# Optimization experiments

Measured on AMD Instinct MI355X. Metric: run time of the kernel, lower is better.

## Reference

```python
import jax, jax.numpy as jnp
import numpy as np

B, C, CI, HM, HC = 4, 64, 32, 128, 64  # batch, in_channels, inter_channels, main HW, cross HW
BN_EPS = 1e-5


def conv1x1(x, w, b):
    # x: [B,Cin,H,W], w: [Cout,Cin], b: [Cout]
    return jnp.einsum('bchw,oc->bohw', x, w) + b[None, :, None, None]


def _lin_coords(n_in, n_out):
    # PyTorch bilinear, align_corners=False: src = (i+0.5)*scale - 0.5, clamped
    scale = n_in / n_out
    src = (jnp.arange(n_out, dtype=jnp.float32) + 0.5) * scale - 0.5
    src = jnp.clip(src, 0.0, n_in - 1)
    i0 = jnp.floor(src).astype(jnp.int32)
    i1 = jnp.minimum(i0 + 1, n_in - 1)
    w = src - i0.astype(jnp.float32)
    return i0, i1, w


def resize_bilinear(x, h_out, w_out):
    # x: [B,C,H,W] -> [B,C,h_out,w_out], matches torch F.interpolate(mode='bilinear', align_corners=False)
    _, _, h_in, w_in = x.shape
    i0, i1, wh = _lin_coords(h_in, h_out)
    x = x[:, :, i0, :] * (1.0 - wh)[None, None, :, None] + x[:, :, i1, :] * wh[None, None, :, None]
    j0, j1, ww = _lin_coords(w_in, w_out)
    x = x[:, :, :, j0] * (1.0 - ww)[None, None, None, :] + x[:, :, :, j1] * ww[None, None, None, :]
    return x


def setup_inputs() -> dict:
    key = jax.random.key(0)
    ks = jax.random.split(key, 12)
    p = lambda k, shape, s=0.05: jax.random.normal(k, shape, dtype=jnp.float32) * s
    return {
        'main_feature': jax.random.normal(ks[0], (B, C, HM, HM), dtype=jnp.float32),
        'cross_feature': jax.random.normal(ks[1], (B, C, HC, HC), dtype=jnp.float32),
        'g_w': p(ks[2], (CI, C)), 'g_b': p(ks[3], (CI,)),
        'theta_w': p(ks[4], (CI, C)), 'theta_b': p(ks[5], (CI,)),
        'phi_w': p(ks[6], (CI, C)), 'phi_b': p(ks[7], (CI,)),
        'w_w': p(ks[8], (C, CI)), 'w_b': p(ks[9], (C,)),
        'bn_gamma': 1.0 + p(ks[10], (C,)), 'bn_beta': p(ks[11], (C,)),
    }


def reference(main_feature, cross_feature, g_w, g_b, theta_w, theta_b,
              phi_w, phi_b, w_w, w_b, bn_gamma, bn_beta):
    b, _, hc, wc = cross_feature.shape
    hm = main_feature.shape[2]
    # g(cross) -> [B, Nc, Ci]
    x = conv1x1(cross_feature, g_w, g_b).reshape(b, CI, -1).transpose(0, 2, 1)
    # theta(cross) -> [B, Ci, Nc]
    y = conv1x1(cross_feature, theta_w, theta_b).reshape(b, CI, -1)
    # phi(resize(main -> cross size)) -> [B, Nc, Ci]
    z = resize_bilinear(main_feature, hc, hc)
    z = conv1x1(z, phi_w, phi_b).reshape(b, CI, -1).transpose(0, 2, 1)
    # unscaled attention: [B, Nc, Nc]
    f = jnp.einsum('bnc,bcm->bnm', x, y)
    attn = jax.nn.softmax(f, axis=-1)
    out = jnp.einsum('bnm,bmc->bnc', attn, z)           # [B, Nc, Ci]
    out = out.transpose(0, 2, 1).reshape(b, CI, hc, wc)  # [B, Ci, Hc, Wc]
    # W: 1x1 conv + BatchNorm2d (training mode: batch statistics, biased var)
    out = conv1x1(out, w_w, w_b)
    mean = out.mean(axis=(0, 2, 3), keepdims=True)
    var = out.var(axis=(0, 2, 3), keepdims=True)
    out = (out - mean) * jax.lax.rsqrt(var + BN_EPS)
    out = out * bn_gamma[None, :, None, None] + bn_beta[None, :, None, None]
    out = resize_bilinear(out, hm, hm)
    return out + main_feature
```

## Files before the change

kernel.cpp:

```cpp
#include <hip/hip_runtime.h>
#include <hip/hip_bf16.h>


typedef __attribute__((ext_vector_type(8))) short bf16x8;
typedef __attribute__((ext_vector_type(4))) float f32x4;
typedef __attribute__((ext_vector_type(16))) float f32x16;

#define LOG2E 1.4426950408889634f

static __device__ __forceinline__ unsigned short f2bf_bits(float x) {
    __hip_bfloat16 h = __float2bfloat16(x);
    return *(unsigned short*)&h;
}
static __device__ __forceinline__ unsigned int pk2bf(float a, float b) {
    __hip_bfloat162 h = __float22bfloat162_rn(make_float2(a, b));
    return *(unsigned int*)&h;
}

static __device__ __forceinline__ void softmax_pack(
    const f32x16& s, float& den, bf16x8& ap1, bf16x8& ap2)
{
    float e[16];
#pragma unroll
    for (int r = 0; r < 16; ++r) e[r] = __builtin_amdgcn_exp2f(s[r]);
    den += (((e[0]+e[1])+(e[2]+e[3])) + ((e[4]+e[5])+(e[6]+e[7])))
         + (((e[8]+e[9])+(e[10]+e[11])) + ((e[12]+e[13])+(e[14]+e[15])));
    uint4 t1 = make_uint4(pk2bf(e[0],e[1]), pk2bf(e[2],e[3]),
                          pk2bf(e[4],e[5]), pk2bf(e[6],e[7]));
    uint4 t2 = make_uint4(pk2bf(e[8],e[9]), pk2bf(e[10],e[11]),
                          pk2bf(e[12],e[13]), pk2bf(e[14],e[15]));
    ap1 = *(bf16x8*)&t1; ap2 = *(bf16x8*)&t2;
}

__global__ __launch_bounds__(256) void qkv_kernel(
    const float* __restrict__ cross, const float* __restrict__ mainf,
    const float* __restrict__ g_w,  const float* __restrict__ g_b,
    const float* __restrict__ th_w, const float* __restrict__ th_b,
    const float* __restrict__ ph_w, const float* __restrict__ ph_b,
    __hip_bfloat16* __restrict__ Qb, __hip_bfloat16* __restrict__ Kf,
    __hip_bfloat16* __restrict__ Vf)
{
    __shared__ float xs[64][128];
    const int kind = blockIdx.x >> 7;
    const int sub  = blockIdx.x & 127;
    const int b    = sub >> 5;
    const int n0   = (sub & 31) << 7;
    const int tid  = threadIdx.x;
    const float* w  = (kind == 0) ? g_w : (kind == 1) ? th_w : ph_w;
    const float* bs = (kind == 0) ? g_b : (kind == 1) ? th_b : ph_b;

    if (kind < 2) {
        const float* src = cross + (((size_t)(b * 64)) << 12) + n0;
        const int jr = (tid & 31) << 2, c0 = tid >> 5;
#pragma unroll
        for (int it = 0; it < 8; ++it) {
            int c = (it << 3) | c0;
            *(float4*)&xs[c][jr] = *(const float4*)(src + ((size_t)c << 12) + jr);
        }
    } else {
        const int px = tid & 127, chh = tid >> 7;
        const int n = n0 + px;
        const int i2 = (n >> 6) << 1, j2 = (n & 63) << 1;
        const float* src = mainf + (((size_t)(b * 64)) << 14) + i2 * 128 + j2;
#pragma unroll 4
        for (int cc = 0; cc < 32; ++cc) {
            int c = (chh << 5) | cc;
            const float2 a = *(const float2*)(src + ((size_t)c << 14));
            const float2 d = *(const float2*)(src + ((size_t)c << 14) + 128);
            xs[c][px] = 0.25f * ((a.x + a.y) + (d.x + d.y));
        }
    }
    __syncthreads();

    const int px = tid & 127, cih = tid >> 7, ci0 = cih << 4;
    float acc[16];
#pragma unroll
    for (int j = 0; j < 16; ++j) acc[j] = bs[ci0 + j];
#pragma unroll 4
    for (int c = 0; c < 64; ++c) {
        float x = xs[c][px];
#pragma unroll
        for (int j = 0; j < 16; ++j)
            acc[j] = fmaf(w[((ci0 + j) << 6) + c], x, acc[j]);
    }
    const int n = n0 + px;
    const int chunk = n >> 5, kk = n & 31;
    if (kind == 0) {
#pragma unroll
        for (int j = 0; j < 16; ++j) acc[j] *= LOG2E;
        unsigned int u[8];
#pragma unroll
        for (int i = 0; i < 8; ++i)
            u[i] = (unsigned int)f2bf_bits(acc[2 * i]) |
                   ((unsigned int)f2bf_bits(acc[2 * i + 1]) << 16);
        uint4* d4 = (uint4*)(Qb + (size_t)((b << 12) + n) * 32 + ci0);
        d4[0] = make_uint4(u[0], u[1], u[2], u[3]);
        d4[1] = make_uint4(u[4], u[5], u[6], u[7]);
    } else if (kind == 1) {
        unsigned int u[8];
#pragma unroll
        for (int i = 0; i < 8; ++i)
            u[i] = (unsigned int)f2bf_bits(acc[2 * i]) |
                   ((unsigned int)f2bf_bits(acc[2 * i + 1]) << 16);
        const int q = (kk & ~12) | ((kk & 4) << 1) | ((kk & 8) >> 1);
        char* base = (char*)Kf + ((((size_t)(b << 7) | chunk) << 11) | (cih << 10));
        *(uint4*)(base + (q << 4))          = make_uint4(u[0], u[1], u[2], u[3]);
        *(uint4*)(base + ((32 + q) << 4))   = make_uint4(u[4], u[5], u[6], u[7]);
    } else {
        const int j = (kk >> 4) & 1, hh = (kk >> 3) & 1, e = kk & 7;
        char* base = (char*)Vf + ((((size_t)(b << 7) | chunk) << 11) | (j << 10) | (e << 1));
#pragma unroll
        for (int jj = 0; jj < 16; ++jj) {
            int ci = ci0 + jj;
            *(unsigned short*)(base + (((hh << 5) | ci) << 4)) = f2bf_bits(acc[jj]);
        }
    }
}

__global__ __launch_bounds__(256) void attn_part(
    const __hip_bfloat16* __restrict__ Qb, const __hip_bfloat16* __restrict__ Kf,
    const __hip_bfloat16* __restrict__ Vf,
    float* __restrict__ pnum, float* __restrict__ pden)
{
    __shared__ __align__(16) float redbuf[4][3][64][20];
    const int tid = threadIdx.x, lane = tid & 63, w = tid >> 6;
    const int q = lane & 31, h = lane >> 5;
    const int b = blockIdx.y, qbase = blockIdx.x << 7, quarter = blockIdx.z;

    const __hip_bfloat16* QrowA = Qb + (((size_t)(b << 12) + qbase + q) << 5);
    const bf16x8 bq1A = *(const bf16x8*)(QrowA + 8 * h);
    const bf16x8 bq2A = *(const bf16x8*)(QrowA + 16 + 8 * h);
    const bf16x8 bq1B = *(const bf16x8*)(QrowA + (32 << 5) + 8 * h);
    const bf16x8 bq2B = *(const bf16x8*)(QrowA + (32 << 5) + 16 + 8 * h);
    const bf16x8 bq1C = *(const bf16x8*)(QrowA + (64 << 5) + 8 * h);
    const bf16x8 bq2C = *(const bf16x8*)(QrowA + (64 << 5) + 16 + 8 * h);
    const bf16x8 bq1D = *(const bf16x8*)(QrowA + (96 << 5) + 8 * h);
    const bf16x8 bq2D = *(const bf16x8*)(QrowA + (96 << 5) + 16 + 8 * h);

    const char* Kc = (const char*)Kf +
        ((size_t)((b << 7) | (quarter << 5) | (w << 3)) << 11) + (lane << 4);
    const char* Vc = (const char*)Vf +
        ((size_t)((b << 7) | (quarter << 5) | (w << 3)) << 11) + (lane << 4);
#define LDK1(c) (*(const bf16x8*)(Kc + ((c) << 11)))
#define LDK2(c) (*(const bf16x8*)(Kc + ((c) << 11) + 1024))
#define LDV1(c) (*(const bf16x8*)(Vc + ((c) << 11)))
#define LDV2(c) (*(const bf16x8*)(Vc + ((c) << 11) + 1024))

    f32x16 accA, accB, accC, accD;
#pragma unroll
    for (int r = 0; r < 16; ++r) { accA[r]=0.f; accB[r]=0.f; accC[r]=0.f; accD[r]=0.f; }
    const f32x16 z16 = accA;
    float denA = 0.f, denB = 0.f, denC = 0.f, denD = 0.f;

    bf16x8 a1c = LDK1(0), a2c = LDK2(0);
    bf16x8 vb1 = LDV1(0), vb2 = LDV2(0);
    bf16x8 a1n = LDK1(1), a2n = LDK2(1);
    bf16x8 vn1 = LDV1(1), vn2 = LDV2(1);
    bf16x8 apA1, apA2, apB1, apB2, apC1, apC2, apD1, apD2, vp1, vp2;

    {
        f32x16 s = __builtin_amdgcn_mfma_f32_32x32x16_bf16(a1c, bq1A, z16, 0, 0, 0);
        s = __builtin_amdgcn_mfma_f32_32x32x16_bf16(a2c, bq2A, s, 0, 0, 0);
        softmax_pack(s, denA, apA1, apA2);
        s = __builtin_amdgcn_mfma_f32_32x32x16_bf16(a1c, bq1B, z16, 0, 0, 0);
        s = __builtin_amdgcn_mfma_f32_32x32x16_bf16(a2c, bq2B, s, 0, 0, 0);
        softmax_pack(s, denB, apB1, apB2);
        s = __builtin_amdgcn_mfma_f32_32x32x16_bf16(a1c, bq1C, z16, 0, 0, 0);
        s = __builtin_amdgcn_mfma_f32_32x32x16_bf16(a2c, bq2C, s, 0, 0, 0);
        softmax_pack(s, denC, apC1, apC2);
        s = __builtin_amdgcn_mfma_f32_32x32x16_bf16(a1c, bq1D, z16, 0, 0, 0);
        s = __builtin_amdgcn_mfma_f32_32x32x16_bf16(a2c, bq2D, s, 0, 0, 0);
        softmax_pack(s, denD, apD1, apD2);
    }

#pragma unroll 2
    for (int ch = 1; ch < 8; ++ch) {
        const int kn = (ch + 1) & 7;
        vp1 = vb1; vp2 = vb2;
        vb1 = vn1; vb2 = vn2;
        a1c = a1n; a2c = a2n;
        a1n = LDK1(kn); a2n = LDK2(kn);
        vn1 = LDV1(kn); vn2 = LDV2(kn);

        accA = __builtin_amdgcn_mfma_f32_32x32x16_bf16(apA1, vp1, accA, 0, 0, 0);
        accA = __builtin_amdgcn_mfma_f32_32x32x16_bf16(apA2, vp2, accA, 0, 0, 0);
        accB = __builtin_amdgcn_mfma_f32_32x32x16_bf16(apB1, vp1, accB, 0, 0, 0);
        accB = __builtin_amdgcn_mfma_f32_32x32x16_bf16(apB2, vp2, accB, 0, 0, 0);
        accC = __builtin_amdgcn_mfma_f32_32x32x16_bf16(apC1, vp1, accC, 0, 0, 0);
        accC = __builtin_amdgcn_mfma_f32_32x32x16_bf16(apC2, vp2, accC, 0, 0, 0);
        accD = __builtin_amdgcn_mfma_f32_32x32x16_bf16(apD1, vp1, accD, 0, 0, 0);
        accD = __builtin_amdgcn_mfma_f32_32x32x16_bf16(apD2, vp2, accD, 0, 0, 0);

        f32x16 s = __builtin_amdgcn_mfma_f32_32x32x16_bf16(a1c, bq1A, z16, 0, 0, 0);
        s = __builtin_amdgcn_mfma_f32_32x32x16_bf16(a2c, bq2A, s, 0, 0, 0);
        softmax_pack(s, denA, apA1, apA2);
        s = __builtin_amdgcn_mfma_f32_32x32x16_bf16(a1c, bq1B, z16, 0, 0, 0);
        s = __builtin_amdgcn_mfma_f32_32x32x16_bf16(a2c, bq2B, s, 0, 0, 0);
        softmax_pack(s, denB, apB1, apB2);
        s = __builtin_amdgcn_mfma_f32_32x32x16_bf16(a1c, bq1C, z16, 0, 0, 0);
        s = __builtin_amdgcn_mfma_f32_32x32x16_bf16(a2c, bq2C, s, 0, 0, 0);
        softmax_pack(s, denC, apC1, apC2);
        s = __builtin_amdgcn_mfma_f32_32x32x16_bf16(a1c, bq1D, z16, 0, 0, 0);
        s = __builtin_amdgcn_mfma_f32_32x32x16_bf16(a2c, bq2D, s, 0, 0, 0);
        softmax_pack(s, denD, apD1, apD2);
    }
    accA = __builtin_amdgcn_mfma_f32_32x32x16_bf16(apA1, vb1, accA, 0, 0, 0);
    accA = __builtin_amdgcn_mfma_f32_32x32x16_bf16(apA2, vb2, accA, 0, 0, 0);
    accB = __builtin_amdgcn_mfma_f32_32x32x16_bf16(apB1, vb1, accB, 0, 0, 0);
    accB = __builtin_amdgcn_mfma_f32_32x32x16_bf16(apB2, vb2, accB, 0, 0, 0);
    accC = __builtin_amdgcn_mfma_f32_32x32x16_bf16(apC1, vb1, accC, 0, 0, 0);
    accC = __builtin_amdgcn_mfma_f32_32x32x16_bf16(apC2, vb2, accC, 0, 0, 0);
    accD = __builtin_amdgcn_mfma_f32_32x32x16_bf16(apD1, vb1, accD, 0, 0, 0);
    accD = __builtin_amdgcn_mfma_f32_32x32x16_bf16(apD2, vb2, accD, 0, 0, 0);
#undef LDK1
#undef LDK2
#undef LDV1
#undef LDV2

    denA += __shfl_xor(denA, 32);
    denB += __shfl_xor(denB, 32);
    denC += __shfl_xor(denC, 32);
    denD += __shfl_xor(denD, 32);

    if (w) {
        float d[4] = {denA, denB, denC, denD};
        const f32x16* av[4] = {&accA, &accB, &accC, &accD};
#pragma unroll
        for (int T = 0; T < 4; ++T) {
            float* rb = &redbuf[T][w - 1][lane][0];
            f32x4* rb4 = (f32x4*)rb;
            const f32x16& a = *av[T];
#pragma unroll
            for (int p = 0; p < 4; ++p) {
                f32x4 t = {a[4*p], a[4*p+1], a[4*p+2], a[4*p+3]};
                rb4[p] = t;
            }
            rb[16] = d[T];
        }
    }
    __syncthreads();
    if (w == 0) {
        const int tbase = (((quarter << 2) | b) << 7) | (blockIdx.x << 2);
        float d[4] = {denA, denB, denC, denD};
        f32x16* av[4] = {&accA, &accB, &accC, &accD};
#pragma unroll
        for (int T = 0; T < 4; ++T) {
            f32x16& a = *av[T];
#pragma unroll
            for (int ww = 0; ww < 3; ++ww) {
                const float* rb = &redbuf[T][ww][lane][0];
                const f32x4* rb4 = (const f32x4*)rb;
#pragma unroll
                for (int p = 0; p < 4; ++p) {
                    f32x4 t = rb4[p];
                    a[4*p] += t[0]; a[4*p+1] += t[1];
                    a[4*p+2] += t[2]; a[4*p+3] += t[3];
                }
                d[T] += rb[16];
            }
            float* pn = pnum + ((size_t)(tbase + T) << 10);
#pragma unroll
            for (int r = 0; r < 16; ++r) {
                int qr = (r & 3) + 8 * (r >> 2) + 4 * h;
                pn[(qr << 5) + q] = a[r];
            }
            if (h == 0) pden[((tbase + T) << 5) + q] = d[T];
        }
    }
}

__global__ __launch_bounds__(256) void attn_combine(
    const float* __restrict__ pnum, const float* __restrict__ pden,
    const float* __restrict__ w_w, const float* __restrict__ w_b,
    float* __restrict__ out2, float2* __restrict__ pstats)
{
    __shared__ __align__(16) float obuf[32][36];
    const int tid = threadIdx.x;
    const int b = blockIdx.y, qbase = blockIdx.x << 5;

#pragma unroll
    for (int k = 0; k < 4; ++k) {
        int e = tid + (k << 8);
        int qr = e >> 5;
        float num = 0.f, den = 0.f;
#pragma unroll
        for (int quarter = 0; quarter < 4; ++quarter) {
            int tile = (((quarter << 2) | b) << 7) | blockIdx.x;
            num += pnum[((size_t)tile << 10) + e];
            den += pden[(tile << 5) + qr];
        }
        obuf[qr][e & 31] = num * (1.0f / den);
    }
    __syncthreads();

    const int qq = tid & 31, cog = tid >> 5;
    float ov[32];
    const float4* orow = (const float4*)&obuf[qq][0];
#pragma unroll
    for (int k4 = 0; k4 < 8; ++k4) {
        float4 t = orow[k4];
        ov[4*k4] = t.x; ov[4*k4+1] = t.y; ov[4*k4+2] = t.z; ov[4*k4+3] = t.w;
    }
    float* dstbase = out2 + (((size_t)(b << 6)) << 12) + qbase + qq;
    const int tileidx = (b << 7) | blockIdx.x;
#pragma unroll
    for (int kk = 0; kk < 8; ++kk) {
        int co = (kk << 3) | cog;
        const float4* wr = (const float4*)&w_w[co << 5];
        float acc2 = w_b[co];
#pragma unroll
        for (int k4 = 0; k4 < 8; ++k4) {
            float4 t = wr[k4];
            acc2 = fmaf(t.x, ov[4*k4],   acc2);
            acc2 = fmaf(t.y, ov[4*k4+1], acc2);
            acc2 = fmaf(t.z, ov[4*k4+2], acc2);
            acc2 = fmaf(t.w, ov[4*k4+3], acc2);
        }
        dstbase[(size_t)co << 12] = acc2;
        float s1 = acc2, s2 = acc2 * acc2;
#pragma unroll
        for (int m = 1; m < 32; m <<= 1) {
            s1 += __shfl_xor(s1, m);
            s2 += __shfl_xor(s2, m);
        }
        if (qq == 0) pstats[(co << 9) | tileidx] = make_float2(s1, s2);
    }
}

__global__ __launch_bounds__(256) void up_kernel(
    const float* __restrict__ out2, const float2* __restrict__ pstats,
    const float* __restrict__ gamma, const float* __restrict__ beta,
    const float* __restrict__ mainf, float* __restrict__ out)
{
    int gid = blockIdx.x * 256 + threadIdx.x;
    int j4 = (gid & 31) << 2;
    int i  = (gid >> 5) & 127;
    int co = (gid >> 12) & 63;
    int b  = gid >> 18;
    int t  = threadIdx.x;

    __shared__ float rs[256], rs2[256];
    {
        float2 p0 = pstats[(co << 9) | t];
        float2 p1 = pstats[(co << 9) | (t + 256)];
        rs[t] = p0.x + p1.x; rs2[t] = p0.y + p1.y;
    }
    __syncthreads();
    for (int off = 128; off > 0; off >>= 1) {
        if (t < off) { rs[t] += rs[t + off]; rs2[t] += rs2[t + off]; }
        __syncthreads();
    }
    float sm = rs[0], sq = rs2[0];

    float mean = sm * (1.0f / 16384.0f);
    float var  = sq * (1.0f / 16384.0f) - mean * mean;
    float inv  = rsqrtf(var + 1e-5f);
    float scale = gamma[co] * inv;
    float shift = beta[co] - mean * scale;

    int ih = i >> 1;
    int k0, k1; float wi;
    if (i & 1)       { k0 = ih;     k1 = (ih < 63) ? ih + 1 : 63; wi = 0.25f; }
    else if (ih == 0){ k0 = 0;      k1 = 0;                       wi = 0.0f;  }
    else             { k0 = ih - 1; k1 = ih;                      wi = 0.75f; }

    const float* p0r = out2 + ((size_t)((b << 6) | co) << 12) + (k0 << 6);
    const float* p1r = out2 + ((size_t)((b << 6) | co) << 12) + (k1 << 6);

    float res[4];
#pragma unroll
    for (int jj = 0; jj < 4; ++jj) {
        int j = j4 | jj;
        int il = j >> 1;
        int l0, l1; float wj;
        if (j & 1)       { l0 = il;     l1 = (il < 63) ? il + 1 : 63; wj = 0.25f; }
        else if (il == 0){ l0 = 0;      l1 = 0;                       wj = 0.0f;  }
        else             { l0 = il - 1; l1 = il;                      wj = 0.75f; }
        float v00 = p0r[l0], v01 = p0r[l1];
        float v10 = p1r[l0], v11 = p1r[l1];
        float top = v00 + wj * (v01 - v00);
        float bot = v10 + wj * (v11 - v10);
        float v = top + wi * (bot - top);
        res[jj] = fmaf(v, scale, shift);
    }
    size_t idx = (((size_t)((b << 6) | co)) << 14) + (i << 7) + j4;
    float4 m4 = *(const float4*)(mainf + idx);
    *(float4*)(out + idx) = make_float4(res[0] + m4.x, res[1] + m4.y,
                                        res[2] + m4.z, res[3] + m4.w);
}

extern "C" void kernel_launch(void* const* d_in, const int* in_sizes, int n_in,
                              void* d_out, int out_size, void* d_ws, size_t ws_size,
                              hipStream_t stream)
{
    const float* mainf = (const float*)d_in[0];
    const float* cross = (const float*)d_in[1];
    const float* g_w   = (const float*)d_in[2];
    const float* g_b   = (const float*)d_in[3];
    const float* th_w  = (const float*)d_in[4];
    const float* th_b  = (const float*)d_in[5];
    const float* ph_w  = (const float*)d_in[6];
    const float* ph_b  = (const float*)d_in[7];
    const float* w_w   = (const float*)d_in[8];
    const float* w_b   = (const float*)d_in[9];
    const float* gamma = (const float*)d_in[10];
    const float* beta  = (const float*)d_in[11];
    float* out = (float*)d_out;

    __hip_bfloat16* Qb = (__hip_bfloat16*)d_ws;
    __hip_bfloat16* Kf = Qb + 524288;
    __hip_bfloat16* Vf = Kf + 524288;
    float* out2   = (float*)(Vf + 524288);
    float* pnum   = out2 + 1048576;
    float* pden   = pnum + 2097152;
    float2* pstats = (float2*)(pden + 65536);

    qkv_kernel<<<384, 256, 0, stream>>>(cross, mainf, g_w, g_b, th_w, th_b,
                                        ph_w, ph_b, Qb, Kf, Vf);
    attn_part<<<dim3(32, 4, 4), 256, 0, stream>>>(Qb, Kf, Vf, pnum, pden);
    attn_combine<<<dim3(128, 4), 256, 0, stream>>>(pnum, pden, w_w, w_b,
                                                   out2, pstats);
    up_kernel<<<4096, 256, 0, stream>>>(out2, pstats, gamma, beta, mainf, out);
}
```

Measured before the change: 143.5 us.

## Compute softmax denominators with MFMA against ones; retile V projection for vector stores

```diff
diff --git a/kernel.cpp b/kernel.cpp
--- a/kernel.cpp
+++ b/kernel.cpp
@@ -18,13 +18,11 @@
 }
 
 static __device__ __forceinline__ void softmax_pack(
-    const f32x16& s, float& den, bf16x8& ap1, bf16x8& ap2)
+    const f32x16& s, bf16x8& ap1, bf16x8& ap2)
 {
     float e[16];
 #pragma unroll
     for (int r = 0; r < 16; ++r) e[r] = __builtin_amdgcn_exp2f(s[r]);
-    den += (((e[0]+e[1])+(e[2]+e[3])) + ((e[4]+e[5])+(e[6]+e[7])))
-         + (((e[8]+e[9])+(e[10]+e[11])) + ((e[12]+e[13])+(e[14]+e[15])));
     uint4 t1 = make_uint4(pk2bf(e[0],e[1]), pk2bf(e[2],e[3]),
                           pk2bf(e[4],e[5]), pk2bf(e[6],e[7]));
     uint4 t2 = make_uint4(pk2bf(e[8],e[9]), pk2bf(e[10],e[11]),
@@ -40,7 +38,7 @@
     __hip_bfloat16* __restrict__ Qb, __hip_bfloat16* __restrict__ Kf,
     __hip_bfloat16* __restrict__ Vf)
 {
-    __shared__ float xs[64][128];
+    __shared__ __align__(16) float xs[64][128];
     const int kind = blockIdx.x >> 7;
     const int sub  = blockIdx.x & 127;
     const int b    = sub >> 5;
@@ -72,48 +70,79 @@
     }
     __syncthreads();
 
-    const int px = tid & 127, cih = tid >> 7, ci0 = cih << 4;
-    float acc[16];
-#pragma unroll
-    for (int j = 0; j < 16; ++j) acc[j] = bs[ci0 + j];
+    if (kind < 2) {
+        const int px = tid & 127, cih = tid >> 7, ci0 = cih << 4;
+        float acc[16];
+#pragma unroll
+        for (int j = 0; j < 16; ++j) acc[j] = bs[ci0 + j];
 #pragma unroll 4
-    for (int c = 0; c < 64; ++c) {
-        float x = xs[c][px];
-#pragma unroll
-        for (int j = 0; j < 16; ++j)
-            acc[j] = fmaf(w[((ci0 + j) << 6) + c], x, acc[j]);
-    }
-    const int n = n0 + px;
-    const int chunk = n >> 5, kk = n & 31;
-    if (kind == 0) {
-#pragma unroll
-        for (int j = 0; j < 16; ++j) acc[j] *= LOG2E;
-        unsigned int u[8];
-#pragma unroll
-        for (int i = 0; i < 8; ++i)
-            u[i] = (unsigned int)f2bf_bits(acc[2 * i]) |
-                   ((unsigned int)f2bf_bits(acc[2 * i + 1]) << 16);
-        uint4* d4 = (uint4*)(Qb + (size_t)((b << 12) + n) * 32 + ci0);
-        d4[0] = make_uint4(u[0], u[1], u[2], u[3]);
-        d4[1] = make_uint4(u[4], u[5], u[6], u[7]);
-    } else if (kind == 1) {
-        unsigned int u[8];
-#pragma unroll
-        for (int i = 0; i < 8; ++i)
-            u[i] = (unsigned int)f2bf_bits(acc[2 * i]) |
-                   ((unsigned int)f2bf_bits(acc[2 * i + 1]) << 16);
-        const int q = (kk & ~12) | ((kk & 4) << 1) | ((kk & 8) >> 1);
-        char* base = (char*)Kf + ((((size_t)(b << 7) | chunk) << 11) | (cih << 10));
-        *(uint4*)(base + (q << 4))          = make_uint4(u[0], u[1], u[2], u[3]);
-        *(uint4*)(base + ((32 + q) << 4))   = make_uint4(u[4], u[5], u[6], u[7]);
+        for (int c = 0; c < 64; ++c) {
+            float x = xs[c][px];
+#pragma unroll
+            for (int j = 0; j < 16; ++j)
+                acc[j] = fmaf(w[((ci0 + j) << 6) + c], x, acc[j]);
+        }
+        const int n = n0 + px;
+        const int chunk = n >> 5, kk = n & 31;
+        if (kind == 0) {
+#pragma unroll
+            for (int j = 0; j < 16; ++j) acc[j] *= LOG2E;
+            unsigned int u[8];
+#pragma unroll
+            for (int i = 0; i < 8; ++i)
+                u[i] = (unsigned int)f2bf_bits(acc[2 * i]) |
+                       ((unsigned int)f2bf_bits(acc[2 * i + 1]) << 16);
+            uint4* d4 = (uint4*)(Qb + (size_t)((b << 12) + n) * 32 + ci0);
+            d4[0] = make_uint4(u[0], u[1], u[2], u[3]);
+            d4[1] = make_uint4(u[4], u[5], u[6], u[7]);
+        } else {
+            unsigned int u[8];
+#pragma unroll
+            for (int i = 0; i < 8; ++i)
+                u[i] = (unsigned int)f2bf_bits(acc[2 * i]) |
+                       ((unsigned int)f2bf_bits(acc[2 * i + 1]) << 16);
+            const int q = (kk & ~12) | ((kk & 4) << 1) | ((kk & 8) >> 1);
+            char* base = (char*)Kf + ((((size_t)(b << 7) | chunk) << 11) | (cih << 10));
+            *(uint4*)(base + (q << 4))          = make_uint4(u[0], u[1], u[2], u[3]);
+            *(uint4*)(base + ((32 + q) << 4))   = make_uint4(u[4], u[5], u[6], u[7]);
+        }
     } else {
-        const int j = (kk >> 4) & 1, hh = (kk >> 3) & 1, e = kk & 7;
-        char* base = (char*)Vf + ((((size_t)(b << 7) | chunk) << 11) | (j << 10) | (e << 1));
-#pragma unroll
-        for (int jj = 0; jj < 16; ++jj) {
-            int ci = ci0 + jj;
-            *(unsigned short*)(base + (((hh << 5) | ci) << 4)) = f2bf_bits(acc[jj]);
-        }
+        const int cip = tid & 15, o = tid >> 4;
+        const int c0 = cip << 1;
+        const int pxb = o << 3;
+        float a0[8], a1[8];
+        const float b0 = bs[c0], b1 = bs[c0 + 1];
+#pragma unroll
+        for (int i = 0; i < 8; ++i) { a0[i] = b0; a1[i] = b1; }
+#pragma unroll 4
+        for (int c = 0; c < 64; ++c) {
+            const float w0 = w[(c0 << 6) + c], w1 = w[((c0 + 1) << 6) + c];
+            const float4 xa = *(const float4*)&xs[c][pxb];
+            const float4 xb = *(const float4*)&xs[c][pxb + 4];
+            a0[0] = fmaf(w0, xa.x, a0[0]); a0[1] = fmaf(w0, xa.y, a0[1]);
+            a0[2] = fmaf(w0, xa.z, a0[2]); a0[3] = fmaf(w0, xa.w, a0[3]);
+            a0[4] = fmaf(w0, xb.x, a0[4]); a0[5] = fmaf(w0, xb.y, a0[5]);
+            a0[6] = fmaf(w0, xb.z, a0[6]); a0[7] = fmaf(w0, xb.w, a0[7]);
+            a1[0] = fmaf(w1, xa.x, a1[0]); a1[1] = fmaf(w1, xa.y, a1[1]);
+            a1[2] = fmaf(w1, xa.z, a1[2]); a1[3] = fmaf(w1, xa.w, a1[3]);
+            a1[4] = fmaf(w1, xb.x, a1[4]); a1[5] = fmaf(w1, xb.y, a1[5]);
+            a1[6] = fmaf(w1, xb.z, a1[6]); a1[7] = fmaf(w1, xb.w, a1[7]);
+        }
+        unsigned int u0[4], u1[4];
+#pragma unroll
+        for (int i = 0; i < 4; ++i) {
+            u0[i] = (unsigned int)f2bf_bits(a0[2 * i]) |
+                    ((unsigned int)f2bf_bits(a0[2 * i + 1]) << 16);
+            u1[i] = (unsigned int)f2bf_bits(a1[2 * i]) |
+                    ((unsigned int)f2bf_bits(a1[2 * i + 1]) << 16);
+        }
+        const int n = n0 + pxb;
+        const int chunk = n >> 5;
+        const int j = (o >> 1) & 1, hh = o & 1;
+        char* base = (char*)Vf + (((size_t)((b << 7) | chunk)) << 11)
+                   + (j << 10) + (hh << 9) + (c0 << 4);
+        *(uint4*)base        = make_uint4(u0[0], u0[1], u0[2], u0[3]);
+        *(uint4*)(base + 16) = make_uint4(u1[0], u1[1], u1[2], u1[3]);
     }
 }
 
@@ -123,6 +152,7 @@
     float* __restrict__ pnum, float* __restrict__ pden)
 {
     __shared__ __align__(16) float redbuf[4][3][64][20];
+    __shared__ __align__(16) float denbuf[4][3][2][16];
     const int tid = threadIdx.x, lane = tid & 63, w = tid >> 6;
     const int q = lane & 31, h = lane >> 5;
     const int b = blockIdx.y, qbase = blockIdx.x << 7, quarter = blockIdx.z;
@@ -137,6 +167,10 @@
     const bf16x8 bq1D = *(const bf16x8*)(QrowA + (96 << 5) + 8 * h);
     const bf16x8 bq2D = *(const bf16x8*)(QrowA + (96 << 5) + 16 + 8 * h);
 
+    bf16x8 ones;
+#pragma unroll
+    for (int i = 0; i < 8; ++i) ones[i] = (short)0x3F80;
+
     const char* Kc = (const char*)Kf +
         ((size_t)((b << 7) | (quarter << 5) | (w << 3)) << 11) + (lane << 4);
     const char* Vc = (const char*)Vf +
@@ -146,11 +180,13 @@
 #define LDV1(c) (*(const bf16x8*)(Vc + ((c) << 11)))
 #define LDV2(c) (*(const bf16x8*)(Vc + ((c) << 11) + 1024))
 
-    f32x16 accA, accB, accC, accD;
-#pragma unroll
-    for (int r = 0; r < 16; ++r) { accA[r]=0.f; accB[r]=0.f; accC[r]=0.f; accD[r]=0.f; }
+    f32x16 accA, accB, accC, accD, dA, dB, dC, dD;
+#pragma unroll
+    for (int r = 0; r < 16; ++r) {
+        accA[r]=0.f; accB[r]=0.f; accC[r]=0.f; accD[r]=0.f;
+        dA[r]=0.f; dB[r]=0.f; dC[r]=0.f; dD[r]=0.f;
+    }
     const f32x16 z16 = accA;
-    float denA = 0.f, denB = 0.f, denC = 0.f, denD = 0.f;
 
     bf16x8 a1c = LDK1(0), a2c = LDK2(0);
     bf16x8 vb1 = LDV1(0), vb2 = LDV2(0);
@@ -161,16 +197,24 @@
     {
         f32x16 s = __builtin_amdgcn_mfma_f32_32x32x16_bf16(a1c, bq1A, z16, 0, 0, 0);
         s = __builtin_amdgcn_mfma_f32_32x32x16_bf16(a2c, bq2A, s, 0, 0, 0);
-        softmax_pack(s, denA, apA1, apA2);
+        softmax_pack(s, apA1, apA2);
+        dA = __builtin_amdgcn_mfma_f32_32x32x16_bf16(apA1, ones, dA, 0, 0, 0);
+        dA = __builtin_amdgcn_mfma_f32_32x32x16_bf16(apA2, ones, dA, 0, 0, 0);
         s = __builtin_amdgcn_mfma_f32_32x32x16_bf16(a1c, bq1B, z16, 0, 0, 0);
         s = __builtin_amdgcn_mfma_f32_32x32x16_bf16(a2c, bq2B, s, 0, 0, 0);
-        softmax_pack(s, denB, apB1, apB2);
+        softmax_pack(s, apB1, apB2);
+        dB = __builtin_amdgcn_mfma_f32_32x32x16_bf16(apB1, ones, dB, 0, 0, 0);
+        dB = __builtin_amdgcn_mfma_f32_32x32x16_bf16(apB2, ones, dB, 0, 0, 0);
         s = __builtin_amdgcn_mfma_f32_32x32x16_bf16(a1c, bq1C, z16, 0, 0, 0);
         s = __builtin_amdgcn_mfma_f32_32x32x16_bf16(a2c, bq2C, s, 0, 0, 0);
-        softmax_pack(s, denC, apC1, apC2);
+        softmax_pack(s, apC1, apC2);
+        dC = __builtin_amdgcn_mfma_f32_32x32x16_bf16(apC1, ones, dC, 0, 0, 0);
+        dC = __builtin_amdgcn_mfma_f32_32x32x16_bf16(apC2, ones, dC, 0, 0, 0);
         s = __builtin_amdgcn_mfma_f32_32x32x16_bf16(a1c, bq1D, z16, 0, 0, 0);
         s = __builtin_amdgcn_mfma_f32_32x32x16_bf16(a2c, bq2D, s, 0, 0, 0);
-        softmax_pack(s, denD, apD1, apD2);
+        softmax_pack(s, apD1, apD2);
+        dD = __builtin_amdgcn_mfma_f32_32x32x16_bf16(apD1, ones, dD, 0, 0, 0);
+        dD = __builtin_amdgcn_mfma_f32_32x32x16_bf16(apD2, ones, dD, 0, 0, 0);
     }
 
 #pragma unroll 2
@@ -193,16 +237,24 @@
 
         f32x16 s = __builtin_amdgcn_mfma_f32_32x32x16_bf16(a1c, bq1A, z16, 0, 0, 0);
         s = __builtin_amdgcn_mfma_f32_32x32x16_bf16(a2c, bq2A, s, 0, 0, 0);
-        softmax_pack(s, denA, apA1, apA2);
+        softmax_pack(s, apA1, apA2);
+        dA = __builtin_amdgcn_mfma_f32_32x32x16_bf16(apA1, ones, dA, 0, 0, 0);
+        dA = __builtin_amdgcn_mfma_f32_32x32x16_bf16(apA2, ones, dA, 0, 0, 0);
         s = __builtin_amdgcn_mfma_f32_32x32x16_bf16(a1c, bq1B, z16, 0, 0, 0);
         s = __builtin_amdgcn_mfma_f32_32x32x16_bf16(a2c, bq2B, s, 0, 0, 0);
-        softmax_pack(s, denB, apB1, apB2);
+        softmax_pack(s, apB1, apB2);
+        dB = __builtin_amdgcn_mfma_f32_32x32x16_bf16(apB1, ones, dB, 0, 0, 0);
+        dB = __builtin_amdgcn_mfma_f32_32x32x16_bf16(apB2, ones, dB, 0, 0, 0);
         s = __builtin_amdgcn_mfma_f32_32x32x16_bf16(a1c, bq1C, z16, 0, 0, 0);
         s = __builtin_amdgcn_mfma_f32_32x32x16_bf16(a2c, bq2C, s, 0, 0, 0);
-        softmax_pack(s, denC, apC1, apC2);
+        softmax_pack(s, apC1, apC2);
+        dC = __builtin_amdgcn_mfma_f32_32x32x16_bf16(apC1, ones, dC, 0, 0, 0);
+        dC = __builtin_amdgcn_mfma_f32_32x32x16_bf16(apC2, ones, dC, 0, 0, 0);
         s = __builtin_amdgcn_mfma_f32_32x32x16_bf16(a1c, bq1D, z16, 0, 0, 0);
         s = __builtin_amdgcn_mfma_f32_32x32x16_bf16(a2c, bq2D, s, 0, 0, 0);
-        softmax_pack(s, denD, apD1, apD2);
+        softmax_pack(s, apD1, apD2);
+        dD = __builtin_amdgcn_mfma_f32_32x32x16_bf16(apD1, ones, dD, 0, 0, 0);
+        dD = __builtin_amdgcn_mfma_f32_32x32x16_bf16(apD2, ones, dD, 0, 0, 0);
     }
     accA = __builtin_amdgcn_mfma_f32_32x32x16_bf16(apA1, vb1, accA, 0, 0, 0);
     accA = __builtin_amdgcn_mfma_f32_32x32x16_bf16(apA2, vb2, accA, 0, 0, 0);
@@ -217,14 +269,9 @@
 #undef LDV1
 #undef LDV2
 
-    denA += __shfl_xor(denA, 32);
-    denB += __shfl_xor(denB, 32);
-    denC += __shfl_xor(denC, 32);
-    denD += __shfl_xor(denD, 32);
-
     if (w) {
-        float d[4] = {denA, denB, denC, denD};
         const f32x16* av[4] = {&accA, &accB, &accC, &accD};
+        const f32x16* dv[4] = {&dA, &dB, &dC, &dD};
 #pragma unroll
         for (int T = 0; T < 4; ++T) {
             float* rb = &redbuf[T][w - 1][lane][0];
@@ -235,17 +282,26 @@
                 f32x4 t = {a[4*p], a[4*p+1], a[4*p+2], a[4*p+3]};
                 rb4[p] = t;
             }
-            rb[16] = d[T];
+            if (q == 0) {
+                const f32x16& d = *dv[T];
+                f32x4* db = (f32x4*)&denbuf[T][w - 1][h][0];
+#pragma unroll
+                for (int p = 0; p < 4; ++p) {
+                    f32x4 t = {d[4*p], d[4*p+1], d[4*p+2], d[4*p+3]};
+                    db[p] = t;
+                }
+            }
         }
     }
     __syncthreads();
     if (w == 0) {
         const int tbase = (((quarter << 2) | b) << 7) | (blockIdx.x << 2);
-        float d[4] = {denA, denB, denC, denD};
         f32x16* av[4] = {&accA, &accB, &accC, &accD};
+        f32x16* dv[4] = {&dA, &dB, &dC, &dD};
 #pragma unroll
         for (int T = 0; T < 4; ++T) {
             f32x16& a = *av[T];
+            f32x16& d = *dv[T];
 #pragma unroll
             for (int ww = 0; ww < 3; ++ww) {
                 const float* rb = &redbuf[T][ww][lane][0];
@@ -256,7 +312,8 @@
                     a[4*p] += t[0]; a[4*p+1] += t[1];
                     a[4*p+2] += t[2]; a[4*p+3] += t[3];
                 }
-                d[T] += rb[16];
+#pragma unroll
+                for (int r = 0; r < 16; ++r) d[r] += denbuf[T][ww][h][r];
             }
             float* pn = pnum + ((size_t)(tbase + T) << 10);
 #pragma unroll
@@ -264,7 +321,13 @@
                 int qr = (r & 3) + 8 * (r >> 2) + 4 * h;
                 pn[(qr << 5) + q] = a[r];
             }
-            if (h == 0) pden[((tbase + T) << 5) + q] = d[T];
+            if (q == 0) {
+#pragma unroll
+                for (int r = 0; r < 16; ++r) {
+                    int qr = (r & 3) + 8 * (r >> 2) + 4 * h;
+                    pden[((tbase + T) << 5) + qr] = d[r];
+                }
+            }
         }
     }
 }
```

New measurement: 147.7 us. +3.0%, slower.

## Split attention keys into eighths and vectorize V projection stores

Applied to the files above, without the earlier changes.

```diff
diff --git a/kernel.cpp b/kernel.cpp
--- a/kernel.cpp
+++ b/kernel.cpp
@@ -40,7 +40,7 @@
     __hip_bfloat16* __restrict__ Qb, __hip_bfloat16* __restrict__ Kf,
     __hip_bfloat16* __restrict__ Vf)
 {
-    __shared__ float xs[64][128];
+    __shared__ __align__(16) float xs[64][128];
     const int kind = blockIdx.x >> 7;
     const int sub  = blockIdx.x & 127;
     const int b    = sub >> 5;
@@ -72,48 +72,79 @@
     }
     __syncthreads();
 
-    const int px = tid & 127, cih = tid >> 7, ci0 = cih << 4;
-    float acc[16];
-#pragma unroll
-    for (int j = 0; j < 16; ++j) acc[j] = bs[ci0 + j];
+    if (kind < 2) {
+        const int px = tid & 127, cih = tid >> 7, ci0 = cih << 4;
+        float acc[16];
+#pragma unroll
+        for (int j = 0; j < 16; ++j) acc[j] = bs[ci0 + j];
 #pragma unroll 4
-    for (int c = 0; c < 64; ++c) {
-        float x = xs[c][px];
-#pragma unroll
-        for (int j = 0; j < 16; ++j)
-            acc[j] = fmaf(w[((ci0 + j) << 6) + c], x, acc[j]);
-    }
-    const int n = n0 + px;
-    const int chunk = n >> 5, kk = n & 31;
-    if (kind == 0) {
-#pragma unroll
-        for (int j = 0; j < 16; ++j) acc[j] *= LOG2E;
-        unsigned int u[8];
-#pragma unroll
-        for (int i = 0; i < 8; ++i)
-            u[i] = (unsigned int)f2bf_bits(acc[2 * i]) |
-                   ((unsigned int)f2bf_bits(acc[2 * i + 1]) << 16);
-        uint4* d4 = (uint4*)(Qb + (size_t)((b << 12) + n) * 32 + ci0);
-        d4[0] = make_uint4(u[0], u[1], u[2], u[3]);
-        d4[1] = make_uint4(u[4], u[5], u[6], u[7]);
-    } else if (kind == 1) {
-        unsigned int u[8];
-#pragma unroll
-        for (int i = 0; i < 8; ++i)
-            u[i] = (unsigned int)f2bf_bits(acc[2 * i]) |
-                   ((unsigned int)f2bf_bits(acc[2 * i + 1]) << 16);
-        const int q = (kk & ~12) | ((kk & 4) << 1) | ((kk & 8) >> 1);
-        char* base = (char*)Kf + ((((size_t)(b << 7) | chunk) << 11) | (cih << 10));
-        *(uint4*)(base + (q << 4))          = make_uint4(u[0], u[1], u[2], u[3]);
-        *(uint4*)(base + ((32 + q) << 4))   = make_uint4(u[4], u[5], u[6], u[7]);
+        for (int c = 0; c < 64; ++c) {
+            float x = xs[c][px];
+#pragma unroll
+            for (int j = 0; j < 16; ++j)
+                acc[j] = fmaf(w[((ci0 + j) << 6) + c], x, acc[j]);
+        }
+        const int n = n0 + px;
+        const int chunk = n >> 5, kk = n & 31;
+        if (kind == 0) {
+#pragma unroll
+            for (int j = 0; j < 16; ++j) acc[j] *= LOG2E;
+            unsigned int u[8];
+#pragma unroll
+            for (int i = 0; i < 8; ++i)
+                u[i] = (unsigned int)f2bf_bits(acc[2 * i]) |
+                       ((unsigned int)f2bf_bits(acc[2 * i + 1]) << 16);
+            uint4* d4 = (uint4*)(Qb + (size_t)((b << 12) + n) * 32 + ci0);
+            d4[0] = make_uint4(u[0], u[1], u[2], u[3]);
+            d4[1] = make_uint4(u[4], u[5], u[6], u[7]);
+        } else {
+            unsigned int u[8];
+#pragma unroll
+            for (int i = 0; i < 8; ++i)
+                u[i] = (unsigned int)f2bf_bits(acc[2 * i]) |
+                       ((unsigned int)f2bf_bits(acc[2 * i + 1]) << 16);
+            const int q = (kk & ~12) | ((kk & 4) << 1) | ((kk & 8) >> 1);
+            char* base = (char*)Kf + ((((size_t)(b << 7) | chunk) << 11) | (cih << 10));
+            *(uint4*)(base + (q << 4))          = make_uint4(u[0], u[1], u[2], u[3]);
+            *(uint4*)(base + ((32 + q) << 4))   = make_uint4(u[4], u[5], u[6], u[7]);
+        }
     } else {
-        const int j = (kk >> 4) & 1, hh = (kk >> 3) & 1, e = kk & 7;
-        char* base = (char*)Vf + ((((size_t)(b << 7) | chunk) << 11) | (j << 10) | (e << 1));
-#pragma unroll
-        for (int jj = 0; jj < 16; ++jj) {
-            int ci = ci0 + jj;
-            *(unsigned short*)(base + (((hh << 5) | ci) << 4)) = f2bf_bits(acc[jj]);
-        }
+        const int cip = tid & 15, o = tid >> 4;
+        const int c0 = cip << 1;
+        const int pxb = o << 3;
+        float a0[8], a1[8];
+        const float b0 = bs[c0], b1 = bs[c0 + 1];
+#pragma unroll
+        for (int i = 0; i < 8; ++i) { a0[i] = b0; a1[i] = b1; }
+#pragma unroll 4
+        for (int c = 0; c < 64; ++c) {
+            const float w0 = w[(c0 << 6) + c], w1 = w[((c0 + 1) << 6) + c];
+            const float4 xa = *(const float4*)&xs[c][pxb];
+            const float4 xb = *(const float4*)&xs[c][pxb + 4];
+            a0[0] = fmaf(w0, xa.x, a0[0]); a0[1] = fmaf(w0, xa.y, a0[1]);
+            a0[2] = fmaf(w0, xa.z, a0[2]); a0[3] = fmaf(w0, xa.w, a0[3]);
+            a0[4] = fmaf(w0, xb.x, a0[4]); a0[5] = fmaf(w0, xb.y, a0[5]);
+            a0[6] = fmaf(w0, xb.z, a0[6]); a0[7] = fmaf(w0, xb.w, a0[7]);
+            a1[0] = fmaf(w1, xa.x, a1[0]); a1[1] = fmaf(w1, xa.y, a1[1]);
+            a1[2] = fmaf(w1, xa.z, a1[2]); a1[3] = fmaf(w1, xa.w, a1[3]);
+            a1[4] = fmaf(w1, xb.x, a1[4]); a1[5] = fmaf(w1, xb.y, a1[5]);
+            a1[6] = fmaf(w1, xb.z, a1[6]); a1[7] = fmaf(w1, xb.w, a1[7]);
+        }
+        unsigned int u0[4], u1[4];
+#pragma unroll
+        for (int i = 0; i < 4; ++i) {
+            u0[i] = (unsigned int)f2bf_bits(a0[2 * i]) |
+                    ((unsigned int)f2bf_bits(a0[2 * i + 1]) << 16);
+            u1[i] = (unsigned int)f2bf_bits(a1[2 * i]) |
+                    ((unsigned int)f2bf_bits(a1[2 * i + 1]) << 16);
+        }
+        const int n = n0 + pxb;
+        const int chunk = n >> 5;
+        const int j = (o >> 1) & 1, hh = o & 1;
+        char* base = (char*)Vf + (((size_t)((b << 7) | chunk)) << 11)
+                   + (j << 10) + (hh << 9) + (c0 << 4);
+        *(uint4*)base        = make_uint4(u0[0], u0[1], u0[2], u0[3]);
+        *(uint4*)(base + 16) = make_uint4(u1[0], u1[1], u1[2], u1[3]);
     }
 }
 
@@ -122,10 +153,11 @@
     const __hip_bfloat16* __restrict__ Vf,
     float* __restrict__ pnum, float* __restrict__ pden)
 {
-    __shared__ __align__(16) float redbuf[4][3][64][20];
+    __shared__ __align__(16) float redbuf[4][3][64][16];
+    __shared__ float denarr[4][3][64];
     const int tid = threadIdx.x, lane = tid & 63, w = tid >> 6;
     const int q = lane & 31, h = lane >> 5;
-    const int b = blockIdx.y, qbase = blockIdx.x << 7, quarter = blockIdx.z;
+    const int b = blockIdx.y, qbase = blockIdx.x << 7, eighth = blockIdx.z;
 
     const __hip_bfloat16* QrowA = Qb + (((size_t)(b << 12) + qbase + q) << 5);
     const bf16x8 bq1A = *(const bf16x8*)(QrowA + 8 * h);
@@ -138,9 +170,9 @@
     const bf16x8 bq2D = *(const bf16x8*)(QrowA + (96 << 5) + 16 + 8 * h);
 
     const char* Kc = (const char*)Kf +
-        ((size_t)((b << 7) | (quarter << 5) | (w << 3)) << 11) + (lane << 4);
+        ((size_t)((b << 7) | (eighth << 4) | (w << 2)) << 11) + (lane << 4);
     const char* Vc = (const char*)Vf +
-        ((size_t)((b << 7) | (quarter << 5) | (w << 3)) << 11) + (lane << 4);
+        ((size_t)((b << 7) | (eighth << 4) | (w << 2)) << 11) + (lane << 4);
 #define LDK1(c) (*(const bf16x8*)(Kc + ((c) << 11)))
 #define LDK2(c) (*(const bf16x8*)(Kc + ((c) << 11) + 1024))
 #define LDV1(c) (*(const bf16x8*)(Vc + ((c) << 11)))
@@ -173,9 +205,9 @@
         softmax_pack(s, denD, apD1, apD2);
     }
 
-#pragma unroll 2
-    for (int ch = 1; ch < 8; ++ch) {
-        const int kn = (ch + 1) & 7;
+#pragma unroll
+    for (int ch = 1; ch < 4; ++ch) {
+        const int kn = (ch + 1) & 3;
         vp1 = vb1; vp2 = vb2;
         vb1 = vn1; vb2 = vn2;
         a1c = a1n; a2c = a2n;
@@ -235,12 +267,12 @@
                 f32x4 t = {a[4*p], a[4*p+1], a[4*p+2], a[4*p+3]};
                 rb4[p] = t;
             }
-            rb[16] = d[T];
+            denarr[T][w - 1][lane] = d[T];
         }
     }
     __syncthreads();
     if (w == 0) {
-        const int tbase = (((quarter << 2) | b) << 7) | (blockIdx.x << 2);
+        const int tbase = (((eighth << 2) | b) << 7) | (blockIdx.x << 2);
         float d[4] = {denA, denB, denC, denD};
         f32x16* av[4] = {&accA, &accB, &accC, &accD};
 #pragma unroll
@@ -256,7 +288,7 @@
                     a[4*p] += t[0]; a[4*p+1] += t[1];
                     a[4*p+2] += t[2]; a[4*p+3] += t[3];
                 }
-                d[T] += rb[16];
+                d[T] += denarr[T][ww][lane];
             }
             float* pn = pnum + ((size_t)(tbase + T) << 10);
 #pragma unroll
@@ -284,8 +316,8 @@
         int qr = e >> 5;
         float num = 0.f, den = 0.f;
 #pragma unroll
-        for (int quarter = 0; quarter < 4; ++quarter) {
-            int tile = (((quarter << 2) | b) << 7) | blockIdx.x;
+        for (int eighth = 0; eighth < 8; ++eighth) {
+            int tile = (((eighth << 2) | b) << 7) | blockIdx.x;
             num += pnum[((size_t)tile << 10) + e];
             den += pden[(tile << 5) + qr];
         }
@@ -412,12 +444,12 @@
     __hip_bfloat16* Vf = Kf + 524288;
     float* out2   = (float*)(Vf + 524288);
     float* pnum   = out2 + 1048576;
-    float* pden   = pnum + 2097152;
-    float2* pstats = (float2*)(pden + 65536);
+    float* pden   = pnum + 4194304;
+    float2* pstats = (float2*)(pden + 131072);
 
     qkv_kernel<<<384, 256, 0, stream>>>(cross, mainf, g_w, g_b, th_w, th_b,
                                         ph_w, ph_b, Qb, Kf, Vf);
-    attn_part<<<dim3(32, 4, 4), 256, 0, stream>>>(Qb, Kf, Vf, pnum, pden);
+    attn_part<<<dim3(32, 4, 8), 256, 0, stream>>>(Qb, Kf, Vf, pnum, pden);
     attn_combine<<<dim3(128, 4), 256, 0, stream>>>(pnum, pden, w_w, w_b,
                                                    out2, pstats);
     up_kernel<<<4096, 256, 0, stream>>>(out2, pstats, gamma, beta, mainf, out);
```

Result: no change. 140.8 us, median of 2 (-1.9%).
